# Kernel optimization log

Hardware: AMD Instinct MI355X
Metric: run time of the kernel (lower is better)

## Reference

```python
import jax, jax.numpy as jnp
import numpy as np

jax.config.update("jax_enable_x64", True)

L_MAX = 9  # matches init_kwargs; K = (L_MAX+1)**2 = 100 modes
SQRT_2_OVER_PI = float(np.sqrt(2.0 / np.pi))


def _l_array(l_max):
    # l repeated 2l+1 times (one entry per (l, m) mode), as float like torch.Tensor
    ls = np.concatenate([np.full(2 * i + 1, i) for i in range(l_max + 1)])
    return jnp.asarray(ls, dtype=jnp.float64)


def _bessel_up(r, k, l_arr, l_max):
    x = r.astype(jnp.float64)[..., None] * k.astype(jnp.float64)  # [N, K]
    j0 = jnp.sin(x) / x
    y = jnp.where(l_arr == 0, j0, 0.0)
    j1 = j0 / x - jnp.cos(x) / x
    y = jnp.where(l_arr == 1, j1, y)
    for i in range(1, l_max):  # small static loop over l (l_max-1 iters)
        j2 = (2 * i + 1) / x * j1 - j0
        y = jnp.where(l_arr == i + 1, j2, y)
        j0, j1 = j1, j2
    y = jnp.where(jnp.abs(x) < 1e-30, 0.0, y)
    y = y * SQRT_2_OVER_PI * k.astype(jnp.float64)
    return y.astype(jnp.float32)


def _bessel_down(r, k, l_arr, l_max):
    x = r.astype(jnp.float64)[..., None] * k.astype(jnp.float64)  # [N, K]
    y = jnp.zeros_like(x)
    lstart = l_max + int(np.sqrt(10 * l_max))
    j2 = jnp.zeros_like(x)
    j1 = jnp.ones_like(x)
    j0 = j1
    for i in range(lstart, 0, -1):  # small static downward recurrence
        j0 = (2 * i + 1) / x * j1 - j2
        if i - 1 < l_max + 1:
            y = jnp.where(l_arr == (i - 1), j0, y)
        j2, j1 = j1, j0
    true_j0 = jnp.sinc(x / jnp.pi)  # = sin(x)/x, matches torch.sinc(r/pi)
    y = y / j0 * true_j0
    small = x < 1e-20
    y = jnp.where(small & (l_arr > 0), 0.0, y)
    y = jnp.where(small & (l_arr == 0), 1.0, y)
    y = y * SQRT_2_OVER_PI * k.astype(jnp.float64)
    return y.astype(jnp.float32)


def setup_inputs() -> dict:
    key = jax.random.key(0)
    k1, k2 = jax.random.split(key)
    N = 262144
    K = (L_MAX + 1) ** 2  # 100
    r = jax.random.uniform(k1, (N,), dtype=jnp.float32, minval=0.1, maxval=20.0)
    k = jax.random.uniform(k2, (K,), dtype=jnp.float32, minval=0.5, maxval=5.0)
    return {"r": r, "k": k}


def reference(r, k):
    l_arr = _l_array(L_MAX)
    up = _bessel_up(r, k, l_arr, L_MAX)    # [N, K] f32
    dn = _bessel_down(r, k, l_arr, L_MAX)  # [N, K] f32
    x32 = r[..., None] * k                 # f32, like the torch forward
    return jnp.where(x32 < l_arr.astype(jnp.float32), dn, up)
```

## Files before the change

kernel.cpp:

```cpp
#include <hip/hip_runtime.h>
#include <math.h>


static constexpr int KMODES = 100;
static constexpr int NTILE  = 64;
static constexpr int TPB    = 4;
static constexpr int TILE_ELEMS = NTILE * KMODES;
static constexpr double PI_D   = 3.14159265358979323846;
static constexpr double BETA_D = 1.0 / (2.0 * PI_D);
static constexpr double S2PI_D = 0.79788456080286535588;

__device__ __forceinline__ float rcpf(float x) { return __builtin_amdgcn_rcpf(x); }
__device__ __forceinline__ float sin_rev(float a) { float r; asm("v_sin_f32 %0, %1" : "=v"(r) : "v"(a)); return r; }
__device__ __forceinline__ float cos_rev(float a) { float r; asm("v_cos_f32 %0, %1" : "=v"(r) : "v"(a)); return r; }

template<int L> struct ZC;
template<> struct ZC<2>{ static constexpr double sg[2]={3,-1};                              static constexpr double gm[1]={-3}; };
template<> struct ZC<3>{ static constexpr double sg[2]={15,-6};                             static constexpr double gm[2]={-15,1}; };
template<> struct ZC<4>{ static constexpr double sg[3]={105,-45,1};                         static constexpr double gm[2]={-105,10}; };
template<> struct ZC<5>{ static constexpr double sg[3]={945,-420,15};                       static constexpr double gm[3]={-945,105,-1}; };
template<> struct ZC<6>{ static constexpr double sg[4]={10395,-4725,210,-1};                static constexpr double gm[3]={-10395,1260,-21}; };
template<> struct ZC<7>{ static constexpr double sg[4]={135135,-62370,3150,-28};            static constexpr double gm[4]={-135135,17325,-378,1}; };
template<> struct ZC<8>{ static constexpr double sg[5]={2027025,-945945,51975,-630,1};      static constexpr double gm[4]={-2027025,270270,-6930,36}; };
template<> struct ZC<9>{ static constexpr double sg[5]={34459425,-16216200,945945,-13860,45}; static constexpr double gm[5]={-34459425,4729725,-135135,990,-1}; };

template<int L> struct WC {
  static constexpr int NS = L / 2 + 1, NG = (L + 1) / 2;
  float sg[NS], gm[NG], xc;
  constexpr WC() : sg{}, gm{}, xc(0.f) {
    constexpr double XT[10] = {0,0,0.088,0.29,0.61,1.01,1.48,2.00,2.55,3.14};
    for (int i = 0; i < NS; ++i) {
      int deg = NS - 1 - i, e = (L & 1) ? (2*deg + 2) : (2*deg + 1);
      double s = S2PI_D; for (int t = 0; t < e; ++t) s *= BETA_D;
      sg[i] = (float)(s * ZC<L>::sg[i]);
    }
    for (int i = 0; i < NG; ++i) {
      int deg = NG - 1 - i, e = (L & 1) ? (2*deg + 1) : (2*deg + 2);
      double s = S2PI_D; for (int t = 0; t < e; ++t) s *= BETA_D;
      gm[i] = (float)(s * ZC<L>::gm[i]);
    }
    xc = (float)(XT[L] * BETA_D);
  }
};

template<int N>
__device__ __forceinline__ float polyH(float y, const float (&a)[N]) {
  float h = a[0];
#pragma unroll
  for (int i = 1; i < N; ++i) h = fmaf(h, y, a[i]);
  return h;
}

struct Flusher {
  const float* src; float* dst; int it; int tid;
  __device__ __forceinline__ void step() {
    if (src != nullptr && it < 7) {
      int e = it * 1024 + tid * 4;
      if (it < 6 || tid < 64) {
        float4 v = *reinterpret_cast<const float4*>(src + e);
        *reinterpret_cast<float4*>(dst + e) = v;
      }
      ++it;
      __builtin_amdgcn_sched_barrier(0);
    }
  }
  __device__ __forceinline__ void finish() {
    if (src != nullptr) { while (it < 7) step(); }
  }
};

template<int L>
__device__ __forceinline__ void do_l(float rvb, const float* __restrict__ kvec,
                                     float* ldsrow, Flusher& fl) {
#pragma unroll
  for (int m = 0; m < 2 * L + 1; ++m) {
    const int KK = L * L + m;
    float kv = kvec[KK];
    float arg = rvb * kv;
    float res;
    if constexpr (L == 0) {
      float w = rcpf(arg);
      res = (sin_rev(arg) * (float)(S2PI_D * BETA_D)) * (kv * w);
    } else if constexpr (L == 1) {
      float w = rcpf(arg);
      float s = sin_rev(arg), c = cos_rev(arg);
      float inner = fmaf(s * w, (float)(S2PI_D * BETA_D * BETA_D),
                         -(c * (float)(S2PI_D * BETA_D)));
      res = (kv * w) * inner;
    } else {
      constexpr WC<L> wc{};
      float argc = fmaxf(arg, wc.xc);
      float w = rcpf(argc);
      float s = sin_rev(argc), c = cos_rev(argc);
      float y = w * w;
      float sgv = polyH(y, wc.sg);
      float gmv = polyH(y, wc.gm);
      float inner;
      if constexpr (L & 1) inner = fmaf(s * w, sgv, c * gmv);
      else                 inner = fmaf(c * w, gmv, s * sgv);
      res = (kv * w) * inner;
    }
    ldsrow[KK] = res;
    if ((m % 3) == 2) fl.step();
  }
}

__global__ __launch_bounds__(256) void sbf_kernel(const float* __restrict__ r,
                                                  const float* __restrict__ kvec,
                                                  float* __restrict__ out) {
  __shared__ float buf[2][TILE_ELEMS];
  const int tid = threadIdx.x;
  const int w = tid >> 6, lane = tid & 63;
  const int tile0 = blockIdx.x * TPB;

  float rvb[TPB];
#pragma unroll
  for (int t = 0; t < TPB; ++t)
    rvb[t] = r[(tile0 + t) * NTILE + lane] * (float)BETA_D;

  Flusher fl{nullptr, nullptr, 7, tid};
#pragma unroll
  for (int t = 0; t < TPB; ++t) {
    float* ldsrow = &buf[t & 1][lane * KMODES];
    if (w == 0)      { do_l<9>(rvb[t], kvec, ldsrow, fl); do_l<2>(rvb[t], kvec, ldsrow, fl); }
    else if (w == 1) { do_l<8>(rvb[t], kvec, ldsrow, fl); do_l<3>(rvb[t], kvec, ldsrow, fl); }
    else if (w == 2) { do_l<7>(rvb[t], kvec, ldsrow, fl); do_l<4>(rvb[t], kvec, ldsrow, fl); do_l<0>(rvb[t], kvec, ldsrow, fl); }
    else             { do_l<6>(rvb[t], kvec, ldsrow, fl); do_l<5>(rvb[t], kvec, ldsrow, fl); do_l<1>(rvb[t], kvec, ldsrow, fl); }
    fl.finish();
    asm volatile("s_waitcnt lgkmcnt(0)" ::: "memory");
    __builtin_amdgcn_s_barrier();
    fl.src = &buf[t & 1][0];
    fl.dst = out + (size_t)(tile0 + t) * TILE_ELEMS;
    fl.it = 0;
  }
  fl.finish();
}

extern "C" void kernel_launch(void* const* d_in, const int* in_sizes, int n_in,
                              void* d_out, int out_size, void* d_ws, size_t ws_size,
                              hipStream_t stream) {
  const float* r = (const float*)d_in[0];
  const float* k = (const float*)d_in[1];
  float* out = (float*)d_out;
  int N = in_sizes[0];
  int blocks = N / NTILE / TPB;
  sbf_kernel<<<blocks, 256, 0, stream>>>(r, k, out);
}
```

Before: 26.18 us.

## Use single-wave blocks computing all modes per row with two-phase LDS flush

Replaces the 256-thread blocks, which split l-groups across four waves and double-buffered four tiles with an interleaved flusher, with 64-thread blocks. Each lane now computes all 100 modes for one radius. Results are staged in LDS in two column halves (52 and 48 columns), and each half is written out with coalesced float4 stores. This drops block-wide barriers and uneven per-wave work, in exchange for losing the overlap of computation with global stores inside a block and running many more, smaller blocks.

```diff
diff --git a/kernel.cpp b/kernel.cpp
--- a/kernel.cpp
+++ b/kernel.cpp
@@ -2,10 +2,6 @@
 #include <math.h>
 
 
-static constexpr int KMODES = 100;
-static constexpr int NTILE  = 64;
-static constexpr int TPB    = 4;
-static constexpr int TILE_ELEMS = NTILE * KMODES;
 static constexpr double PI_D   = 3.14159265358979323846;
 static constexpr double BETA_D = 1.0 / (2.0 * PI_D);
 static constexpr double S2PI_D = 0.79788456080286535588;
@@ -51,89 +47,92 @@
   return h;
 }
 
-struct Flusher {
-  const float* src; float* dst; int it; int tid;
-  __device__ __forceinline__ void step() {
-    if (src != nullptr && it < 7) {
-      int e = it * 1024 + tid * 4;
-      if (it < 6 || tid < 64) {
-        float4 v = *reinterpret_cast<const float4*>(src + e);
-        *reinterpret_cast<float4*>(dst + e) = v;
-      }
-      ++it;
-      __builtin_amdgcn_sched_barrier(0);
-    }
-  }
-  __device__ __forceinline__ void finish() {
-    if (src != nullptr) { while (it < 7) step(); }
-  }
-};
-
 template<int L>
-__device__ __forceinline__ void do_l(float rvb, const float* __restrict__ kvec,
-                                     float* ldsrow, Flusher& fl) {
-#pragma unroll
-  for (int m = 0; m < 2 * L + 1; ++m) {
-    const int KK = L * L + m;
-    float kv = kvec[KK];
-    float arg = rvb * kv;
-    float res;
-    if constexpr (L == 0) {
-      float w = rcpf(arg);
-      res = (sin_rev(arg) * (float)(S2PI_D * BETA_D)) * (kv * w);
-    } else if constexpr (L == 1) {
-      float w = rcpf(arg);
-      float s = sin_rev(arg), c = cos_rev(arg);
-      float inner = fmaf(s * w, (float)(S2PI_D * BETA_D * BETA_D),
-                         -(c * (float)(S2PI_D * BETA_D)));
-      res = (kv * w) * inner;
-    } else {
-      constexpr WC<L> wc{};
-      float argc = fmaxf(arg, wc.xc);
-      float w = rcpf(argc);
-      float s = sin_rev(argc), c = cos_rev(argc);
-      float y = w * w;
-      float sgv = polyH(y, wc.sg);
-      float gmv = polyH(y, wc.gm);
-      float inner;
-      if constexpr (L & 1) inner = fmaf(s * w, sgv, c * gmv);
-      else                 inner = fmaf(c * w, gmv, s * sgv);
-      res = (kv * w) * inner;
-    }
-    ldsrow[KK] = res;
-    if ((m % 3) == 2) fl.step();
+__device__ __forceinline__ float mode_val(float rvb, float kv) {
+  float arg = rvb * kv;
+  if constexpr (L == 0) {
+    float w = rcpf(arg);
+    return (sin_rev(arg) * (float)(S2PI_D * BETA_D)) * (kv * w);
+  } else if constexpr (L == 1) {
+    float w = rcpf(arg);
+    float s = sin_rev(arg), c = cos_rev(arg);
+    float inner = fmaf(s * w, (float)(S2PI_D * BETA_D * BETA_D),
+                       -(c * (float)(S2PI_D * BETA_D)));
+    return (kv * w) * inner;
+  } else {
+    constexpr WC<L> wc{};
+    float argc = fmaxf(arg, wc.xc);
+    float w = rcpf(argc);
+    float s = sin_rev(argc), c = cos_rev(argc);
+    float y = w * w;
+    float sgv = polyH(y, wc.sg);
+    float gmv = polyH(y, wc.gm);
+    float inner;
+    if constexpr (L & 1) inner = fmaf(s * w, sgv, c * gmv);
+    else                 inner = fmaf(c * w, gmv, s * sgv);
+    return (kv * w) * inner;
   }
 }
 
-__global__ __launch_bounds__(256) void sbf_kernel(const float* __restrict__ r,
-                                                  const float* __restrict__ kvec,
-                                                  float* __restrict__ out) {
-  __shared__ float buf[2][TILE_ELEMS];
-  const int tid = threadIdx.x;
-  const int w = tid >> 6, lane = tid & 63;
-  const int tile0 = blockIdx.x * TPB;
+template<int L, int MLO, int MHI, int KKB>
+__device__ __forceinline__ void do_lr(float rvb, const float* __restrict__ kvec,
+                                      float* rowbase) {
+#pragma unroll
+  for (int m = MLO; m < MHI; ++m) {
+    const int KK = L * L + m;
+    rowbase[KK - KKB] = mode_val<L>(rvb, kvec[KK]);
+  }
+}
 
-  float rvb[TPB];
+template<int W, int CB, int ROUNDS>
+__device__ __forceinline__ void flushW(const float* __restrict__ lds,
+                                       float* __restrict__ outrow, int lane) {
+  int e = lane * 4;
+  int n = e / W;
+  int c = e - n * W;
+  const float* lp = lds + e;
+  float* gp = outrow + n * 100 + CB + c;
+  constexpr int DN = 256 / W, DC = 256 % W;
 #pragma unroll
-  for (int t = 0; t < TPB; ++t)
-    rvb[t] = r[(tile0 + t) * NTILE + lane] * (float)BETA_D;
+  for (int rnd = 0; rnd < ROUNDS; ++rnd) {
+    float4 v = *reinterpret_cast<const float4*>(lp);
+    *reinterpret_cast<float4*>(gp) = v;
+    lp += 256;
+    c += DC;
+    bool carry = (c >= W);
+    c = carry ? (c - W) : c;
+    gp += DN * 100 + DC + (carry ? (100 - W) : 0);
+  }
+}
 
-  Flusher fl{nullptr, nullptr, 7, tid};
-#pragma unroll
-  for (int t = 0; t < TPB; ++t) {
-    float* ldsrow = &buf[t & 1][lane * KMODES];
-    if (w == 0)      { do_l<9>(rvb[t], kvec, ldsrow, fl); do_l<2>(rvb[t], kvec, ldsrow, fl); }
-    else if (w == 1) { do_l<8>(rvb[t], kvec, ldsrow, fl); do_l<3>(rvb[t], kvec, ldsrow, fl); }
-    else if (w == 2) { do_l<7>(rvb[t], kvec, ldsrow, fl); do_l<4>(rvb[t], kvec, ldsrow, fl); do_l<0>(rvb[t], kvec, ldsrow, fl); }
-    else             { do_l<6>(rvb[t], kvec, ldsrow, fl); do_l<5>(rvb[t], kvec, ldsrow, fl); do_l<1>(rvb[t], kvec, ldsrow, fl); }
-    fl.finish();
-    asm volatile("s_waitcnt lgkmcnt(0)" ::: "memory");
-    __builtin_amdgcn_s_barrier();
-    fl.src = &buf[t & 1][0];
-    fl.dst = out + (size_t)(tile0 + t) * TILE_ELEMS;
-    fl.it = 0;
+__global__ __launch_bounds__(64) void sbf_kernel(const float* __restrict__ r,
+                                                 const float* __restrict__ kvec,
+                                                 float* __restrict__ out) {
+  __shared__ float lds[64 * 52];
+  const int lane = threadIdx.x;
+  const int n0 = blockIdx.x * 64;
+  float rvb = r[n0 + lane] * (float)BETA_D;
+  float* outrow = out + (size_t)n0 * 100;
+
+  {
+    float* rowbase = lds + lane * 52;
+    do_lr<0, 0,  1, 0>(rvb, kvec, rowbase);
+    do_lr<1, 0,  3, 0>(rvb, kvec, rowbase);
+    do_lr<2, 0,  5, 0>(rvb, kvec, rowbase);
+    do_lr<3, 0,  7, 0>(rvb, kvec, rowbase);
+    do_lr<4, 0,  9, 0>(rvb, kvec, rowbase);
+    do_lr<5, 0, 11, 0>(rvb, kvec, rowbase);
+    do_lr<6, 0, 13, 0>(rvb, kvec, rowbase);
+    do_lr<7, 0,  3, 0>(rvb, kvec, rowbase);
+    flushW<52, 0, 13>(lds, outrow, lane);
   }
-  fl.finish();
+  {
+    float* rowbase = lds + lane * 48;
+    do_lr<7, 3, 15, 52>(rvb, kvec, rowbase);
+    do_lr<8, 0, 17, 52>(rvb, kvec, rowbase);
+    do_lr<9, 0, 19, 52>(rvb, kvec, rowbase);
+    flushW<48, 52, 12>(lds, outrow, lane);
+  }
 }
 
 extern "C" void kernel_launch(void* const* d_in, const int* in_sizes, int n_in,
@@ -143,6 +142,6 @@
   const float* k = (const float*)d_in[1];
   float* out = (float*)d_out;
   int N = in_sizes[0];
-  int blocks = N / NTILE / TPB;
-  sbf_kernel<<<blocks, 256, 0, stream>>>(r, k, out);
+  int blocks = N / 64;
+  sbf_kernel<<<blocks, 64, 0, stream>>>(r, k, out);
 }
```

New measurement: 29.56 us. +12.9%, slower.
